# Optimization experiments

Hardware: AMD Instinct MI355X
Metric: run time of the kernel (lower is better)

Reference implementation:

```python
import jax, jax.numpy as jnp
import numpy as np

B, GRID, N, C, S = 2, 128, 100000, 64, 2

def setup_inputs() -> dict:
    key = jax.random.key(0)
    k1, k2, k3 = jax.random.split(key, 3)
    # unique sparse voxel coordinates in a (B, GRID^3) grid
    lin = jax.random.permutation(k1, B * GRID ** 3)[:N].astype(jnp.int32)
    b = lin // GRID ** 3
    r = lin % GRID ** 3
    x = r // GRID ** 2
    y = (r // GRID) % GRID
    z = r % GRID
    coords = jnp.stack([b, x, y, z], axis=-1)  # [N,4] int32
    feats = jax.random.normal(k2, (N, C), dtype=jnp.float32)
    default_feat = 0.1 * jax.random.normal(k3, (C,), dtype=jnp.float32)
    return {"coords": coords, "feats": feats, "default_feat": default_feat}

def reference(coords, feats, default_feat):
    n, c = feats.shape
    s = S
    b = coords[:, 0]
    xyz = coords[:, 1:]
    # --- output coordinates: each coarse voxel expands to an s^3 fine block ---
    ar = jnp.arange(s, dtype=jnp.int32)
    offs = jnp.stack(jnp.meshgrid(ar, ar, ar, indexing="ij"), axis=-1).reshape(-1, 3)  # [s^3,3]
    out_xyz = (xyz[:, None, :] * s + offs[None, :, :]).reshape(-1, 3)  # [N*s^3,3]
    out_b = jnp.repeat(b, s ** 3)  # [N*s^3]
    # --- map fine voxel centers back to coarse space (align_corners=False) ---
    src = (out_xyz.astype(feats.dtype) + 0.5) / s - 0.5
    f0f = jnp.floor(src)
    frac = src - f0f  # [M,3] trilinear fractions
    f0 = f0f.astype(jnp.int32)
    # --- hash table: sorted linearized coarse keys ---
    key_in = ((b * GRID + xyz[:, 0]) * GRID + xyz[:, 1]) * GRID + xyz[:, 2]
    order = jnp.argsort(key_in)
    keys_sorted = key_in[order]
    feats_sorted = feats[order]
    acc = jnp.zeros((out_xyz.shape[0], c), dtype=feats.dtype)
    for corner in range(8):  # fixed 8-corner loop (not a data-dim loop)
        d = jnp.array([(corner >> 2) & 1, (corner >> 1) & 1, corner & 1], dtype=jnp.int32)
        nb = f0 + d[None, :]  # [M,3] neighbor coarse coords
        w = jnp.prod(jnp.where(d[None, :] == 1, frac, 1.0 - frac), axis=-1)  # [M]
        valid = jnp.all((nb >= 0) & (nb < GRID), axis=-1)
        nbc = jnp.clip(nb, 0, GRID - 1)
        qkey = ((out_b * GRID + nbc[:, 0]) * GRID + nbc[:, 1]) * GRID + nbc[:, 2]
        idx = jnp.clip(jnp.searchsorted(keys_sorted, qkey), 0, n - 1)
        found = valid & (keys_sorted[idx] == qkey)
        g = jnp.where(found[:, None], feats_sorted[idx], default_feat[None, :])
        acc = acc + w[:, None] * g
    return acc  # [N*s^3, C] upsampled features (paired with out_b/out_xyz coords)
```

## Files before the change

### kernel.cpp

```cpp
#include <hip/hip_runtime.h>

#define G 128
#define BITMAP_BYTES (2u * G * G * G / 8u)

__global__ void build_kernel(const int4* __restrict__ coords,
                             unsigned* __restrict__ bitmap,
                             int* __restrict__ table, int n) {
    int i = blockIdx.x * blockDim.x + threadIdx.x;
    if (i >= n) return;
    int4 c = coords[i];
    int key = (c.x << 21) | (c.y << 14) | (c.z << 7) | c.w;
    table[key] = i;
    atomicOr(&bitmap[key >> 5], 1u << (key & 31));
}

__global__ void upsample_kernel(const int4* __restrict__ coords,
                                const float4* __restrict__ feats,
                                const float4* __restrict__ dflt,
                                const unsigned* __restrict__ bitmap,
                                const int* __restrict__ table,
                                float4* __restrict__ out,
                                int n) {
    int t = blockIdx.x * blockDim.x + threadIdx.x;
    int i = t >> 4;
    int cg = t & 15;
    if (i >= n) return;
    int4 c = coords[i];
    int b = c.x, x = c.y, y = c.z, z = c.w;
    float4 d = dflt[cg];
    float4 f = feats[(size_t)i * 16 + cg];
    float4 base;
    base.x = d.x + 0.421875f * (f.x - d.x);
    base.y = d.y + 0.421875f * (f.y - d.y);
    base.z = d.z + 0.421875f * (f.z - d.z);
    base.w = d.w + 0.421875f * (f.w - d.w);
    float4 acc[8];
    #pragma unroll
    for (int o = 0; o < 8; ++o) acc[o] = base;

    int bbase = b << 21;
    #pragma unroll
    for (int ei = 0; ei < 27; ++ei) {
        if (ei == 13) continue;
        const int ex = ei / 9 - 1;
        const int ey = (ei / 3) % 3 - 1;
        const int ez = ei % 3 - 1;
        int nx = x + ex, ny = y + ey, nz = z + ez;
        bool valid = ((unsigned)nx < G) & ((unsigned)ny < G) & ((unsigned)nz < G);
        int key = bbase | ((nx & (G - 1)) << 14) | ((ny & (G - 1)) << 7) | (nz & (G - 1));
        unsigned wrd = bitmap[key >> 5];
        if (valid && ((wrd >> (key & 31)) & 1u)) {
            int idx = table[key];
            float4 g = feats[(size_t)idx * 16 + cg];
            const float w = ((ex == 0) ? 0.75f : 0.25f) *
                            ((ey == 0) ? 0.75f : 0.25f) *
                            ((ez == 0) ? 0.75f : 0.25f);
            float4 delta;
            delta.x = w * (g.x - d.x);
            delta.y = w * (g.y - d.y);
            delta.z = w * (g.z - d.z);
            delta.w = w * (g.w - d.w);
            const int x0 = (ex == 1) ? 1 : 0, x1 = (ex == -1) ? 0 : 1;
            const int y0 = (ey == 1) ? 1 : 0, y1 = (ey == -1) ? 0 : 1;
            const int z0 = (ez == 1) ? 1 : 0, z1 = (ez == -1) ? 0 : 1;
            #pragma unroll
            for (int ox = x0; ox <= x1; ++ox)
                #pragma unroll
                for (int oy = y0; oy <= y1; ++oy)
                    #pragma unroll
                    for (int oz = z0; oz <= z1; ++oz) {
                        int o = ox * 4 + oy * 2 + oz;
                        acc[o].x += delta.x;
                        acc[o].y += delta.y;
                        acc[o].z += delta.z;
                        acc[o].w += delta.w;
                    }
        }
    }
    size_t rbase = ((size_t)i * 8) * 16 + cg;
    #pragma unroll
    for (int o = 0; o < 8; ++o) out[rbase + o * 16] = acc[o];
}

extern "C" void kernel_launch(void* const* d_in, const int* in_sizes, int n_in,
                              void* d_out, int out_size, void* d_ws, size_t ws_size,
                              hipStream_t stream) {
    const int4*   coords = (const int4*)d_in[0];
    const float4* feats  = (const float4*)d_in[1];
    const float4* dflt   = (const float4*)d_in[2];
    float4*       out    = (float4*)d_out;
    int n = in_sizes[0] / 4;

    unsigned* bitmap = (unsigned*)d_ws;
    int* table = (int*)((char*)d_ws + BITMAP_BYTES);

    hipMemsetAsync(bitmap, 0, BITMAP_BYTES, stream);
    build_kernel<<<(n + 255) / 256, 256, 0, stream>>>(coords, bitmap, table, n);

    long long total = (long long)n * 16;
    int blocks = (int)((total + 255) / 256);
    upsample_kernel<<<blocks, 256, 0, stream>>>(coords, feats, dflt, bitmap, table, out, n);
}
```

Baseline: 290.4 us.

## Distribute neighbor hash lookups across lanes and broadcast hits via ballot/shuffle

Each point is handled by 16 lanes, one per channel group. Previously every lane repeated all 26 neighbor bitmap and table lookups. Now each of the 16 lanes probes at most two neighbors, packs the hit's feature index and its 8-output mask into one word, and the group walks the ballot of hits, broadcasting each packed hit with a shuffle. This removes redundant per-lane address math, loads and divergent branches, since hits are sparse. The cost is extra ballot and shuffle traffic, a data-dependent loop over hits, and multiply-by-mask accumulation into all 8 outputs per hit.

```diff
diff --git a/kernel.cpp b/kernel.cpp
--- a/kernel.cpp
+++ b/kernel.cpp
@@ -14,70 +14,96 @@
     atomicOr(&bitmap[key >> 5], 1u << (key & 31));
 }
 
-__global__ void upsample_kernel(const int4* __restrict__ coords,
-                                const float4* __restrict__ feats,
-                                const float4* __restrict__ dflt,
-                                const unsigned* __restrict__ bitmap,
-                                const int* __restrict__ table,
-                                float4* __restrict__ out,
-                                int n) {
+#define APPLY_HIT(p)                                                        \
+    {                                                                       \
+        int idx = (int)((p) >> 8) - 1;                                      \
+        unsigned om = (p) & 255u;                                           \
+        int pc = __popc(om);                                                \
+        float w = (pc == 4) ? 0.140625f : ((pc == 2) ? 0.046875f : 0.015625f); \
+        float4 g4 = feats[(size_t)idx * 16 + cg];                           \
+        float ddx = w * (g4.x - d4.x), ddy = w * (g4.y - d4.y);             \
+        float ddz = w * (g4.z - d4.z), ddw = w * (g4.w - d4.w);             \
+        _Pragma("unroll")                                                   \
+        for (int o = 0; o < 8; ++o) {                                       \
+            float s = (float)((om >> o) & 1u);                              \
+            acc[o].x += s * ddx; acc[o].y += s * ddy;                       \
+            acc[o].z += s * ddz; acc[o].w += s * ddw;                       \
+        }                                                                   \
+    }
+
+__global__ __launch_bounds__(256) void upsample_kernel(
+        const int4* __restrict__ coords,
+        const float4* __restrict__ feats,
+        const float4* __restrict__ dflt,
+        const unsigned* __restrict__ bitmap,
+        const int* __restrict__ table,
+        float4* __restrict__ out,
+        int n) {
     int t = blockIdx.x * blockDim.x + threadIdx.x;
     int i = t >> 4;
     int cg = t & 15;
     if (i >= n) return;
+    int lane = threadIdx.x & 63;
+    int g = lane >> 4;
+    int l = lane & 15;
+
     int4 c = coords[i];
-    int b = c.x, x = c.y, y = c.z, z = c.w;
-    float4 d = dflt[cg];
-    float4 f = feats[(size_t)i * 16 + cg];
+    int x = c.y, y = c.z, z = c.w;
+    int bbase = c.x << 21;
+
+    unsigned packed0 = 0u, packed1 = 0u;
+    if (l < 13) {
+        #pragma unroll
+        for (int r = 0; r < 2; ++r) {
+            int di = l + (r ? 14 : 0);
+            int ex = di / 9 - 1;
+            int ey = (di / 3) % 3 - 1;
+            int ez = di % 3 - 1;
+            int nx = x + ex, ny = y + ey, nz = z + ez;
+            bool valid = ((unsigned)nx < G) & ((unsigned)ny < G) & ((unsigned)nz < G);
+            int key = valid ? (bbase | (nx << 14) | (ny << 7) | nz) : bbase;
+            unsigned wrd = bitmap[key >> 5];
+            unsigned p = 0u;
+            if (valid && ((wrd >> (key & 31)) & 1u)) {
+                int idx = table[key];
+                unsigned xm = (ex == 0) ? 3u : ((ex < 0) ? 1u : 2u);
+                unsigned ym = (ey == 0) ? 3u : ((ey < 0) ? 1u : 2u);
+                unsigned zm = (ez == 0) ? 3u : ((ez < 0) ? 1u : 2u);
+                unsigned myz = ((ym & 1u) ? zm : 0u) | ((ym & 2u) ? (zm << 2) : 0u);
+                unsigned om  = ((xm & 1u) ? myz : 0u) | ((xm & 2u) ? (myz << 4) : 0u);
+                p = ((unsigned)(idx + 1) << 8) | om;
+            }
+            if (r) packed1 = p; else packed0 = p;
+        }
+    }
+    unsigned long long bal0 = __ballot(packed0 != 0u);
+    unsigned long long bal1 = __ballot(packed1 != 0u);
+
+    float4 d4 = dflt[cg];
+    float4 f4 = feats[(size_t)i * 16 + cg];
     float4 base;
-    base.x = d.x + 0.421875f * (f.x - d.x);
-    base.y = d.y + 0.421875f * (f.y - d.y);
-    base.z = d.z + 0.421875f * (f.z - d.z);
-    base.w = d.w + 0.421875f * (f.w - d.w);
+    base.x = d4.x + 0.421875f * (f4.x - d4.x);
+    base.y = d4.y + 0.421875f * (f4.y - d4.y);
+    base.z = d4.z + 0.421875f * (f4.z - d4.z);
+    base.w = d4.w + 0.421875f * (f4.w - d4.w);
     float4 acc[8];
     #pragma unroll
     for (int o = 0; o < 8; ++o) acc[o] = base;
 
-    int bbase = b << 21;
-    #pragma unroll
-    for (int ei = 0; ei < 27; ++ei) {
-        if (ei == 13) continue;
-        const int ex = ei / 9 - 1;
-        const int ey = (ei / 3) % 3 - 1;
-        const int ez = ei % 3 - 1;
-        int nx = x + ex, ny = y + ey, nz = z + ez;
-        bool valid = ((unsigned)nx < G) & ((unsigned)ny < G) & ((unsigned)nz < G);
-        int key = bbase | ((nx & (G - 1)) << 14) | ((ny & (G - 1)) << 7) | (nz & (G - 1));
-        unsigned wrd = bitmap[key >> 5];
-        if (valid && ((wrd >> (key & 31)) & 1u)) {
-            int idx = table[key];
-            float4 g = feats[(size_t)idx * 16 + cg];
-            const float w = ((ex == 0) ? 0.75f : 0.25f) *
-                            ((ey == 0) ? 0.75f : 0.25f) *
-                            ((ez == 0) ? 0.75f : 0.25f);
-            float4 delta;
-            delta.x = w * (g.x - d.x);
-            delta.y = w * (g.y - d.y);
-            delta.z = w * (g.z - d.z);
-            delta.w = w * (g.w - d.w);
-            const int x0 = (ex == 1) ? 1 : 0, x1 = (ex == -1) ? 0 : 1;
-            const int y0 = (ey == 1) ? 1 : 0, y1 = (ey == -1) ? 0 : 1;
-            const int z0 = (ez == 1) ? 1 : 0, z1 = (ez == -1) ? 0 : 1;
-            #pragma unroll
-            for (int ox = x0; ox <= x1; ++ox)
-                #pragma unroll
-                for (int oy = y0; oy <= y1; ++oy)
-                    #pragma unroll
-                    for (int oz = z0; oz <= z1; ++oz) {
-                        int o = ox * 4 + oy * 2 + oz;
-                        acc[o].x += delta.x;
-                        acc[o].y += delta.y;
-                        acc[o].z += delta.z;
-                        acc[o].w += delta.w;
-                    }
-        }
+    unsigned m0 = (unsigned)((bal0 >> (g * 16)) & 0x1FFFull);
+    unsigned m1 = (unsigned)((bal1 >> (g * 16)) & 0x1FFFull);
+    while (m0) {
+        int j = __ffs(m0) - 1; m0 &= m0 - 1;
+        unsigned p = (unsigned)__shfl((int)packed0, (g << 4) + j, 64);
+        APPLY_HIT(p);
     }
-    size_t rbase = ((size_t)i * 8) * 16 + cg;
+    while (m1) {
+        int j = __ffs(m1) - 1; m1 &= m1 - 1;
+        unsigned p = (unsigned)__shfl((int)packed1, (g << 4) + j, 64);
+        APPLY_HIT(p);
+    }
+
+    size_t rbase = (size_t)i * 128 + cg;
     #pragma unroll
     for (int o = 0; o < 8; ++o) out[rbase + o * 16] = acc[o];
 }
```

After: 257.4 us. 1.13x faster.
